# Optimization experiments

Measured on AMD Instinct MI355X. Metric: run time of the kernel, lower is better.

The kernel has to match this reference:

```python
import jax, jax.numpy as jnp
import numpy as np

G = 100000   # num graphs
N = 2000000  # num nodes
E = 4000000  # num edges (unused downstream, kept for fidelity)
D = 300      # emb_dim
L = 50       # num noise levels


def setup_inputs() -> dict:
    key = jax.random.key(0)
    ks = jax.random.split(key, 12)
    node2graph = jnp.sort(jax.random.randint(ks[0], (N,), 0, G))
    edge_index = jax.random.randint(ks[1], (2, E), 0, N)
    noise_level = jax.random.randint(ks[2], (G,), 0, L)
    molecule_repr = jax.random.normal(ks[3], (G, D), dtype=jnp.float32)
    pos_noise_pred = jax.random.normal(ks[4], (N, 3), dtype=jnp.float32)
    pos_perturbed = jax.random.normal(ks[5], (N, 3), dtype=jnp.float32)
    pos_target = jax.random.normal(ks[6], (N, 3), dtype=jnp.float32)
    s = 1.0 / np.sqrt(D)
    W1 = jax.random.uniform(ks[7], (D, D), minval=-s, maxval=s, dtype=jnp.float32)
    b1 = jax.random.uniform(ks[8], (D,), minval=-s, maxval=s, dtype=jnp.float32)
    W2 = jax.random.uniform(ks[9], (D, D), minval=-s, maxval=s, dtype=jnp.float32)
    b2 = jax.random.uniform(ks[10], (D,), minval=-s, maxval=s, dtype=jnp.float32)
    sigmas = jnp.asarray(np.exp(np.linspace(np.log(10.0), np.log(0.01), L)), dtype=jnp.float32)
    return dict(node2graph=node2graph, edge_index=edge_index, noise_level=noise_level,
                num_graphs=G, molecule_repr=molecule_repr, pos_noise_pred=pos_noise_pred,
                pos_perturbed=pos_perturbed, pos_target=pos_target,
                W1=W1, b1=b1, W2=W2, b2=b2, sigmas=sigmas)


def _score_target_riemann(pos_perturbed, pos_target, node2graph, num_graphs):
    # @torch.no_grad() branch: all scatter_mean/scatter_add indexed by node2graph
    seg_sum = lambda x: jax.ops.segment_sum(x, node2graph, num_segments=num_graphs)
    cnt = jnp.maximum(seg_sum(jnp.ones((node2graph.shape[0],), jnp.float32)), 1.0)[:, None]
    center = seg_sum(pos_target) / cnt                 # [G,3]
    p_center = seg_sum(pos_perturbed) / cnt            # [G,3]
    pos_c = pos_target - center[node2graph]            # [N,3]
    pp_c = pos_perturbed - p_center[node2graph]        # [N,3]
    # per-graph 3x3 matrices: ptp[i,j] = sum pp_i*pp_j, otp[i,j] = sum pos_c_i*pp_j
    ptp = seg_sum(pp_c[:, :, None] * pp_c[:, None, :])   # [G,3,3]
    otp = seg_sum(pos_c[:, :, None] * pp_c[:, None, :])  # [G,3,3]
    ptp_n = ptp[node2graph]                              # [N,3,3]
    otp_n = otp[node2graph]                              # [N,3,3]
    num = -2.0 * (jnp.einsum('ni,nij->nj', pp_c, ptp_n)
                  - jnp.einsum('ni,nij->nj', pos_c, otp_n))  # [N,3]
    den = (jnp.linalg.norm(ptp_n.reshape(-1, 9), axis=-1)
           + jnp.linalg.norm(otp_n.reshape(-1, 9), axis=-1))[:, None]
    return num / den


def reference(node2graph, edge_index, noise_level, num_graphs, molecule_repr,
              pos_noise_pred, pos_perturbed, pos_target, W1, b1, W2, b2, sigmas):
    edge2graph = node2graph[edge_index[0]]  # computed but unused, as in original
    used_sigmas = sigmas[noise_level][node2graph][:, None]  # [N,1]
    score_target = jax.lax.stop_gradient(
        _score_target_riemann(pos_perturbed, pos_target, node2graph, num_graphs)
    ) / used_sigmas
    pred_noise = (pos_noise_pred - pos_perturbed) * (1.0 / used_sigmas)
    per_node = jnp.sum((pred_noise - score_target) ** 2, axis=-1)  # [N]
    per_graph = jax.ops.segment_sum(per_node, node2graph, num_segments=num_graphs)
    pos_denoise = per_graph.mean()
    # noise-level prediction head: Linear -> SiLU -> Linear, CE over noise_level
    h = jax.nn.silu(molecule_repr @ W1 + b1)
    logits = h @ W2 + b2  # [G,D]
    logp = jax.nn.log_softmax(logits, axis=-1)
    ce = -jnp.take_along_axis(logp, noise_level[:, None], axis=1)[:, 0]
    loss_pred_noise = ce.mean()
    return jnp.stack([pos_denoise, loss_pred_noise])
```

## Files before the change

kernel.cpp:

```cpp
#include <hip/hip_runtime.h>
#include <math.h>


typedef __attribute__((ext_vector_type(8))) short bf16x8;
typedef __attribute__((ext_vector_type(4))) short s16x4;
typedef __attribute__((ext_vector_type(4))) float f32x4;

__device__ __forceinline__ short bt(float f) {
    return (short)(__float_as_uint(f) >> 16);
}

#define TM   64
#define DRL  300
#define DP   320
#define XS   328
#define NT   20
#define MT   4
#define KCH  10


__global__ __launch_bounds__(256)
void k_bnd(const int* __restrict__ n2g, int* __restrict__ gs,
           int* __restrict__ ge, int N) {
    int t = blockIdx.x * blockDim.x + threadIdx.x;
    if (t >= N) return;
    int g = n2g[t];
    if (t == 0     || n2g[t - 1] != g) gs[g] = t;
    if (t == N - 1 || n2g[t + 1] != g) ge[g] = t + 1;
}

__global__ __launch_bounds__(256)
void k_graph(const int* __restrict__ gs, const int* __restrict__ ge,
             const float* __restrict__ pt, const float* __restrict__ pp,
             const float* __restrict__ pnp,
             const int* __restrict__ nl, const float* __restrict__ sigmas,
             double* __restrict__ accA, int G) {
    const int tg = blockIdx.x * blockDim.x + threadIdx.x;
    const int g  = tg >> 2;
    const int j  = tg & 3;
    float q = 0.f;
    if (g < G) {
        const int s = gs[g], e = ge[g];
        float st0=0,st1=0,st2=0, sp0=0,sp1=0,sp2=0;
        float m00=0,m01=0,m02=0,m11=0,m12=0,m22=0;
        float t00=0,t01=0,t02=0,t10=0,t11=0,t12=0,t20=0,t21=0,t22=0;
        for (int i = s + j; i < e; i += 4) {
            float a0 = pt[3*i], a1 = pt[3*i+1], a2 = pt[3*i+2];
            float b0 = pp[3*i], b1 = pp[3*i+1], b2 = pp[3*i+2];
            st0 += a0; st1 += a1; st2 += a2;
            sp0 += b0; sp1 += b1; sp2 += b2;
            m00 += b0*b0; m01 += b0*b1; m02 += b0*b2;
            m11 += b1*b1; m12 += b1*b2; m22 += b2*b2;
            t00 += a0*b0; t01 += a0*b1; t02 += a0*b2;
            t10 += a1*b0; t11 += a1*b1; t12 += a1*b2;
            t20 += a2*b0; t21 += a2*b1; t22 += a2*b2;
        }
#define QR(x) do { x += __shfl_xor(x, 1, 64); x += __shfl_xor(x, 2, 64); } while (0)
        QR(st0); QR(st1); QR(st2); QR(sp0); QR(sp1); QR(sp2);
        QR(m00); QR(m01); QR(m02); QR(m11); QR(m12); QR(m22);
        QR(t00); QR(t01); QR(t02); QR(t10); QR(t11); QR(t12);
        QR(t20); QR(t21); QR(t22);
#undef QR
        float cnt = fmaxf((float)(e - s), 1.f);
        float ic  = 1.f / cnt;
        float c0 = st0 * ic, c1 = st1 * ic, c2 = st2 * ic;
        float d0 = sp0 * ic, d1 = sp1 * ic, d2 = sp2 * ic;
        float p00 = m00 - cnt*d0*d0, p01 = m01 - cnt*d0*d1;
        float p02 = m02 - cnt*d0*d2, p11 = m11 - cnt*d1*d1;
        float p12 = m12 - cnt*d1*d2, p22 = m22 - cnt*d2*d2;
        float o00 = t00 - cnt*c0*d0, o01 = t01 - cnt*c0*d1, o02 = t02 - cnt*c0*d2;
        float o10 = t10 - cnt*c1*d0, o11 = t11 - cnt*c1*d1, o12 = t12 - cnt*c1*d2;
        float o20 = t20 - cnt*c2*d0, o21 = t21 - cnt*c2*d1, o22 = t22 - cnt*c2*d2;
        float ptn = sqrtf(p00*p00 + p11*p11 + p22*p22 +
                          2.f*(p01*p01 + p02*p02 + p12*p12));
        float otn = sqrtf(o00*o00 + o01*o01 + o02*o02 +
                          o10*o10 + o11*o11 + o12*o12 +
                          o20*o20 + o21*o21 + o22*o22);
        float den = ptn + otn;
        float idn = (den > 0.f) ? (1.f / den) : 0.f;
        float sg  = sigmas[nl[g]];
        float is2 = 1.f / (sg * sg);
        for (int i = s + j; i < e; i += 4) {
            float a0 = pt[3*i] - c0, a1 = pt[3*i+1] - c1, a2 = pt[3*i+2] - c2;
            float bb0 = pp[3*i],  bb1 = pp[3*i+1],  bb2 = pp[3*i+2];
            float b0 = bb0 - d0, b1 = bb1 - d1, b2 = bb2 - d2;
            float n0 = -2.f * ((b0*p00 + b1*p01 + b2*p02) - (a0*o00 + a1*o10 + a2*o20));
            float n1 = -2.f * ((b0*p01 + b1*p11 + b2*p12) - (a0*o01 + a1*o11 + a2*o21));
            float n2 = -2.f * ((b0*p02 + b1*p12 + b2*p22) - (a0*o02 + a1*o12 + a2*o22));
            float e0 = (pnp[3*i]   - bb0) - n0 * idn;
            float e1 = (pnp[3*i+1] - bb1) - n1 * idn;
            float e2 = (pnp[3*i+2] - bb2) - n2 * idn;
            q += (e0*e0 + e1*e1 + e2*e2) * is2;
        }
    }
    for (int o = 32; o > 0; o >>= 1) q += __shfl_down(q, o, 64);
    if ((threadIdx.x & 63) == 0)
        atomicAdd(&accA[(blockIdx.x * 4 + (threadIdx.x >> 6)) & 255], (double)q);
}


__global__ void k_prepw(const float* __restrict__ W1, const float* __restrict__ W2,
                        short* __restrict__ Wb1, short* __restrict__ Wb2) {
    int id = blockIdx.x * blockDim.x + threadIdx.x;
    if (id >= 2 * DP * DP) return;
    int mat = id / (DP * DP);
    int rem = id - mat * DP * DP;
    int k = rem / DP, n = rem - (rem / DP) * DP;
    const float* W = mat ? W2 : W1;
    short* Wb = mat ? Wb2 : Wb1;
    float v = (k < DRL && n < DRL) ? W[k * DRL + n] : 0.f;
    int kc = k >> 5, kin = k & 31, quad = kin >> 3, j = kin & 7;
    int t = n >> 4, l16 = n & 15;
    Wb[(((kc * NT + t) * 64) + quad * 16 + l16) * 8 + j] = bt(v);
}


__global__ __launch_bounds__(640, 5)
void k_mlp(const float* __restrict__ X,
           const short* __restrict__ Wb1, const short* __restrict__ Wb2,
           const float* __restrict__ b1, const float* __restrict__ b2,
           const int* __restrict__ nl,
           double* __restrict__ accC, int G) {
    __shared__ __align__(16) short Xs[TM * XS];

    const int tid  = threadIdx.x;
    const int wv   = tid >> 6;
    const int lane = tid & 63;
    const int quad = lane >> 4;
    const int l16  = lane & 15;
    const int m0   = blockIdx.x * TM;

    const float4* Xv = (const float4*)X;
    for (int idx = tid; idx < TM * 75; idx += 640) {
        int r = idx / 75, c = idx - r * 75;
        int gr = m0 + r;
        float4 v = {0.f, 0.f, 0.f, 0.f};
        if (gr < G) v = Xv[gr * 75 + c];
        s16x4 sv = { bt(v.x), bt(v.y), bt(v.z), bt(v.w) };
        *(s16x4*)&Xs[r * XS + c * 4] = sv;
    }
    for (int idx = tid; idx < TM * (DP - DRL); idx += 640) {
        int r = idx / (DP - DRL), c = idx - r * (DP - DRL);
        Xs[r * XS + DRL + c] = 0;
    }
    __syncthreads();

    const bf16x8* B1 = (const bf16x8*)Wb1;
    const bf16x8* B2 = (const bf16x8*)Wb2;
    const int tile0 = wv * 2, tile1 = wv * 2 + 1;

    f32x4 acc[MT][2];
    const f32x4 vzero = {0.f, 0.f, 0.f, 0.f};
#pragma unroll
    for (int m = 0; m < MT; ++m) { acc[m][0] = vzero; acc[m][1] = vzero; }

    bf16x8 nb0 = B1[(0 * NT + tile0) * 64 + lane];
    bf16x8 nb1 = B1[(0 * NT + tile1) * 64 + lane];
#pragma unroll
    for (int kc = 0; kc < KCH; ++kc) {
        bf16x8 b0v = nb0, b1v = nb1;
        if (kc + 1 < KCH) {
            nb0 = B1[((kc + 1) * NT + tile0) * 64 + lane];
            nb1 = B1[((kc + 1) * NT + tile1) * 64 + lane];
        }
        bf16x8 a[MT];
#pragma unroll
        for (int m = 0; m < MT; ++m)
            a[m] = *(const bf16x8*)&Xs[(m * 16 + l16) * XS + kc * 32 + quad * 8];
#pragma unroll
        for (int m = 0; m < MT; ++m) {
            acc[m][0] = __builtin_amdgcn_mfma_f32_16x16x32_bf16(a[m], b0v, acc[m][0], 0, 0, 0);
            acc[m][1] = __builtin_amdgcn_mfma_f32_16x16x32_bf16(a[m], b1v, acc[m][1], 0, 0, 0);
        }
    }
    __syncthreads();

#pragma unroll
    for (int t = 0; t < 2; ++t) {
        int col = (wv * 2 + t) * 16 + l16;
        float bias = (col < DRL) ? b1[col] : 0.f;
#pragma unroll
        for (int m = 0; m < MT; ++m)
#pragma unroll
            for (int r = 0; r < 4; ++r) {
                float v = acc[m][t][r] + bias;
                float h = v / (1.f + __expf(-v));
                Xs[(m * 16 + quad * 4 + r) * XS + col] = bt(h);
            }
    }
    __syncthreads();

#pragma unroll
    for (int m = 0; m < MT; ++m) { acc[m][0] = vzero; acc[m][1] = vzero; }
    nb0 = B2[(0 * NT + tile0) * 64 + lane];
    nb1 = B2[(0 * NT + tile1) * 64 + lane];
#pragma unroll
    for (int kc = 0; kc < KCH; ++kc) {
        bf16x8 b0v = nb0, b1v = nb1;
        if (kc + 1 < KCH) {
            nb0 = B2[((kc + 1) * NT + tile0) * 64 + lane];
            nb1 = B2[((kc + 1) * NT + tile1) * 64 + lane];
        }
        bf16x8 a[MT];
#pragma unroll
        for (int m = 0; m < MT; ++m)
            a[m] = *(const bf16x8*)&Xs[(m * 16 + l16) * XS + kc * 32 + quad * 8];
#pragma unroll
        for (int m = 0; m < MT; ++m) {
            acc[m][0] = __builtin_amdgcn_mfma_f32_16x16x32_bf16(a[m], b0v, acc[m][0], 0, 0, 0);
            acc[m][1] = __builtin_amdgcn_mfma_f32_16x16x32_bf16(a[m], b1v, acc[m][1], 0, 0, 0);
        }
    }
    __syncthreads();

    float* S = (float*)Xs;
    float* T = S + TM * 10;
    const int colA = tile0 * 16 + l16;
    const int colB = tile1 * 16 + l16;
    const float biasA = (colA < DRL) ? b2[colA] : 0.f;
    const float biasB = (colB < DRL) ? b2[colB] : 0.f;
#pragma unroll
    for (int m = 0; m < MT; ++m) {
#pragma unroll
        for (int r = 0; r < 4; ++r) {
            int row = m * 16 + quad * 4 + r;
            int grow = m0 + row;
            int ct = (grow < G) ? nl[grow] : -1;
            float lgA = acc[m][0][r] + biasA;
            float lgB = acc[m][1][r] + biasB;
            float sw = ((colA < DRL) ? __expf(lgA) : 0.f) +
                       ((colB < DRL) ? __expf(lgB) : 0.f);
            for (int o = 1; o < 16; o <<= 1) sw += __shfl_xor(sw, o, 64);
            if (l16 == 0) S[row * 10 + wv] = sw;
            if (colA == ct) T[row] = lgA;
            if (colB == ct) T[row] = lgB;
        }
    }
    __syncthreads();
    if (tid < 64) {
        int row = tid;
        int grow = m0 + row;
        float q = 0.f;
        if (grow < G) {
            float ss = 0.f;
#pragma unroll
            for (int w = 0; w < 10; ++w) ss += S[row * 10 + w];
            q = __logf(ss) - T[row];
        }
        for (int o = 32; o > 0; o >>= 1) q += __shfl_down(q, o, 64);
        if (tid == 0) atomicAdd(&accC[blockIdx.x & 255], (double)q);
    }
}


__global__ void k_final(const double* __restrict__ accA,
                        const double* __restrict__ accC,
                        float* __restrict__ out, float invG) {
    int t = threadIdx.x;
    double a = accA[t] + accA[t + 64] + accA[t + 128] + accA[t + 192];
    double c = accC[t] + accC[t + 64] + accC[t + 128] + accC[t + 192];
    for (int o = 32; o > 0; o >>= 1) {
        a += __shfl_down(a, o, 64);
        c += __shfl_down(c, o, 64);
    }
    if (t == 0) {
        out[0] = (float)(a * (double)invG);
        out[1] = (float)(c * (double)invG);
    }
}


extern "C" void kernel_launch(void* const* d_in, const int* in_sizes, int n_in,
                              void* d_out, int out_size, void* d_ws, size_t ws_size,
                              hipStream_t stream) {
    const int*   n2g = (const int*)d_in[0];
    const int*   nl  = (const int*)d_in[2];
    const float* X   = (const float*)d_in[4];
    const float* pnp = (const float*)d_in[5];
    const float* pp  = (const float*)d_in[6];
    const float* pt  = (const float*)d_in[7];
    const float* W1  = (const float*)d_in[8];
    const float* b1  = (const float*)d_in[9];
    const float* W2  = (const float*)d_in[10];
    const float* b2  = (const float*)d_in[11];
    const float* sig = (const float*)d_in[12];

    const int N = in_sizes[0];
    const int G = in_sizes[2];

    double* accA = (double*)d_ws;
    double* accC = accA + 256;
    short*  Wb1  = (short*)((char*)d_ws + 4096);
    short*  Wb2  = Wb1 + DP * DP;
    int*    gs   = (int*)((char*)d_ws + 4096 + (size_t)2 * DP * DP * 2);
    int*    ge   = gs + G;

    hipMemsetAsync(d_ws, 0, 4096, stream);
    hipMemsetAsync(gs, 0, (size_t)2 * G * 4, stream);

    k_prepw<<<(2 * DP * DP + 255) / 256, 256, 0, stream>>>(W1, W2, Wb1, Wb2);
    k_bnd<<<(N + 255) / 256, 256, 0, stream>>>(n2g, gs, ge, N);
    k_graph<<<(4 * G + 255) / 256, 256, 0, stream>>>(gs, ge, pt, pp, pnp,
                                                     nl, sig, accA, G);
    k_mlp<<<(G + TM - 1) / TM, 640, 0, stream>>>(X, Wb1, Wb2, b1, b2, nl,
                                                 accC, G);
    k_final<<<1, 64, 0, stream>>>(accA, accC, (float*)d_out, 1.0f / (float)G);
}
```

Before: 395.2 us.

## Vectorize graph kernel loads and retile MLP to 32-row blocks of 4 waves

The per-graph kernel now loads positions as aligned float4 groups covering four nodes, masking nodes outside the graph, instead of strided scalar loads. The MLP kernel is retiled to 32-row blocks with 256 threads, where each wave computes five column tiles over two row tiles. The aims are better memory coalescing and higher occupancy. In exchange, weight traffic per row doubles and boundary groups are loaded redundantly.

```diff
diff --git a/kernel.cpp b/kernel.cpp
--- a/kernel.cpp
+++ b/kernel.cpp
@@ -10,12 +10,12 @@
     return (short)(__float_as_uint(f) >> 16);
 }
 
-#define TM   64
+#define TM   32
 #define DRL  300
 #define DP   320
 #define XS   328
 #define NT   20
-#define MT   4
+#define NW   5
 #define KCH  10
 
 
@@ -41,19 +41,39 @@
     float q = 0.f;
     if (g < G) {
         const int s = gs[g], e = ge[g];
+        const int g0 = s >> 2, g1 = (e + 3) >> 2;
+        const float4* ptv = (const float4*)pt;
+        const float4* ppv = (const float4*)pp;
+        const float4* pnv = (const float4*)pnp;
         float st0=0,st1=0,st2=0, sp0=0,sp1=0,sp2=0;
         float m00=0,m01=0,m02=0,m11=0,m12=0,m22=0;
         float t00=0,t01=0,t02=0,t10=0,t11=0,t12=0,t20=0,t21=0,t22=0;
-        for (int i = s + j; i < e; i += 4) {
-            float a0 = pt[3*i], a1 = pt[3*i+1], a2 = pt[3*i+2];
-            float b0 = pp[3*i], b1 = pp[3*i+1], b2 = pp[3*i+2];
-            st0 += a0; st1 += a1; st2 += a2;
-            sp0 += b0; sp1 += b1; sp2 += b2;
-            m00 += b0*b0; m01 += b0*b1; m02 += b0*b2;
-            m11 += b1*b1; m12 += b1*b2; m22 += b2*b2;
-            t00 += a0*b0; t01 += a0*b1; t02 += a0*b2;
-            t10 += a1*b0; t11 += a1*b1; t12 += a1*b2;
-            t20 += a2*b0; t21 += a2*b1; t22 += a2*b2;
+        for (int gg = g0 + j; gg < g1; gg += 4) {
+            float4 x0 = ptv[3*gg], x1 = ptv[3*gg+1], x2 = ptv[3*gg+2];
+            float4 y0 = ppv[3*gg], y1 = ppv[3*gg+1], y2 = ppv[3*gg+2];
+            float A[12] = {x0.x,x0.y,x0.z,x0.w, x1.x,x1.y,x1.z,x1.w,
+                           x2.x,x2.y,x2.z,x2.w};
+            float B[12] = {y0.x,y0.y,y0.z,y0.w, y1.x,y1.y,y1.z,y1.w,
+                           y2.x,y2.y,y2.z,y2.w};
+            const int base = gg * 4;
+#pragma unroll
+            for (int k = 0; k < 4; ++k) {
+                const int i = base + k;
+                const bool v = (i >= s) && (i < e);
+                float a0 = v ? A[3*k+0] : 0.f;
+                float a1 = v ? A[3*k+1] : 0.f;
+                float a2 = v ? A[3*k+2] : 0.f;
+                float b0 = v ? B[3*k+0] : 0.f;
+                float b1 = v ? B[3*k+1] : 0.f;
+                float b2 = v ? B[3*k+2] : 0.f;
+                st0 += a0; st1 += a1; st2 += a2;
+                sp0 += b0; sp1 += b1; sp2 += b2;
+                m00 += b0*b0; m01 += b0*b1; m02 += b0*b2;
+                m11 += b1*b1; m12 += b1*b2; m22 += b2*b2;
+                t00 += a0*b0; t01 += a0*b1; t02 += a0*b2;
+                t10 += a1*b0; t11 += a1*b1; t12 += a1*b2;
+                t20 += a2*b0; t21 += a2*b1; t22 += a2*b2;
+            }
         }
 #define QR(x) do { x += __shfl_xor(x, 1, 64); x += __shfl_xor(x, 2, 64); } while (0)
         QR(st0); QR(st1); QR(st2); QR(sp0); QR(sp1); QR(sp2);
@@ -80,17 +100,33 @@
         float idn = (den > 0.f) ? (1.f / den) : 0.f;
         float sg  = sigmas[nl[g]];
         float is2 = 1.f / (sg * sg);
-        for (int i = s + j; i < e; i += 4) {
-            float a0 = pt[3*i] - c0, a1 = pt[3*i+1] - c1, a2 = pt[3*i+2] - c2;
-            float bb0 = pp[3*i],  bb1 = pp[3*i+1],  bb2 = pp[3*i+2];
-            float b0 = bb0 - d0, b1 = bb1 - d1, b2 = bb2 - d2;
-            float n0 = -2.f * ((b0*p00 + b1*p01 + b2*p02) - (a0*o00 + a1*o10 + a2*o20));
-            float n1 = -2.f * ((b0*p01 + b1*p11 + b2*p12) - (a0*o01 + a1*o11 + a2*o21));
-            float n2 = -2.f * ((b0*p02 + b1*p12 + b2*p22) - (a0*o02 + a1*o12 + a2*o22));
-            float e0 = (pnp[3*i]   - bb0) - n0 * idn;
-            float e1 = (pnp[3*i+1] - bb1) - n1 * idn;
-            float e2 = (pnp[3*i+2] - bb2) - n2 * idn;
-            q += (e0*e0 + e1*e1 + e2*e2) * is2;
+        for (int gg = g0 + j; gg < g1; gg += 4) {
+            float4 x0 = ptv[3*gg], x1 = ptv[3*gg+1], x2 = ptv[3*gg+2];
+            float4 y0 = ppv[3*gg], y1 = ppv[3*gg+1], y2 = ppv[3*gg+2];
+            float4 z0 = pnv[3*gg], z1 = pnv[3*gg+1], z2 = pnv[3*gg+2];
+            float A[12] = {x0.x,x0.y,x0.z,x0.w, x1.x,x1.y,x1.z,x1.w,
+                           x2.x,x2.y,x2.z,x2.w};
+            float B[12] = {y0.x,y0.y,y0.z,y0.w, y1.x,y1.y,y1.z,y1.w,
+                           y2.x,y2.y,y2.z,y2.w};
+            float C[12] = {z0.x,z0.y,z0.z,z0.w, z1.x,z1.y,z1.z,z1.w,
+                           z2.x,z2.y,z2.z,z2.w};
+            const int base = gg * 4;
+#pragma unroll
+            for (int k = 0; k < 4; ++k) {
+                const int i = base + k;
+                const bool v = (i >= s) && (i < e);
+                float a0 = A[3*k+0] - c0, a1 = A[3*k+1] - c1, a2 = A[3*k+2] - c2;
+                float bb0 = B[3*k+0], bb1 = B[3*k+1], bb2 = B[3*k+2];
+                float b0 = bb0 - d0, b1 = bb1 - d1, b2 = bb2 - d2;
+                float n0 = -2.f * ((b0*p00 + b1*p01 + b2*p02) - (a0*o00 + a1*o10 + a2*o20));
+                float n1 = -2.f * ((b0*p01 + b1*p11 + b2*p12) - (a0*o01 + a1*o11 + a2*o21));
+                float n2 = -2.f * ((b0*p02 + b1*p12 + b2*p22) - (a0*o02 + a1*o12 + a2*o22));
+                float e0 = (C[3*k+0] - bb0) - n0 * idn;
+                float e1 = (C[3*k+1] - bb1) - n1 * idn;
+                float e2 = (C[3*k+2] - bb2) - n2 * idn;
+                float contrib = (e0*e0 + e1*e1 + e2*e2) * is2;
+                q += v ? contrib : 0.f;
+            }
         }
     }
     for (int o = 32; o > 0; o >>= 1) q += __shfl_down(q, o, 64);
@@ -115,7 +151,7 @@
 }
 
 
-__global__ __launch_bounds__(640, 5)
+__global__ __launch_bounds__(256, 4)
 void k_mlp(const float* __restrict__ X,
            const short* __restrict__ Wb1, const short* __restrict__ Wb2,
            const float* __restrict__ b1, const float* __restrict__ b2,
@@ -129,9 +165,10 @@
     const int quad = lane >> 4;
     const int l16  = lane & 15;
     const int m0   = blockIdx.x * TM;
+    const int tb0  = wv * NW;
 
     const float4* Xv = (const float4*)X;
-    for (int idx = tid; idx < TM * 75; idx += 640) {
+    for (int idx = tid; idx < TM * 75; idx += 256) {
         int r = idx / 75, c = idx - r * 75;
         int gr = m0 + r;
         float4 v = {0.f, 0.f, 0.f, 0.f};
@@ -139,7 +176,7 @@
         s16x4 sv = { bt(v.x), bt(v.y), bt(v.z), bt(v.w) };
         *(s16x4*)&Xs[r * XS + c * 4] = sv;
     }
-    for (int idx = tid; idx < TM * (DP - DRL); idx += 640) {
+    for (int idx = tid; idx < TM * (DP - DRL); idx += 256) {
         int r = idx / (DP - DRL), c = idx - r * (DP - DRL);
         Xs[r * XS + DRL + c] = 0;
     }
@@ -147,43 +184,48 @@
 
     const bf16x8* B1 = (const bf16x8*)Wb1;
     const bf16x8* B2 = (const bf16x8*)Wb2;
-    const int tile0 = wv * 2, tile1 = wv * 2 + 1;
-
-    f32x4 acc[MT][2];
+
+    f32x4 acc[2][NW];
     const f32x4 vzero = {0.f, 0.f, 0.f, 0.f};
 #pragma unroll
-    for (int m = 0; m < MT; ++m) { acc[m][0] = vzero; acc[m][1] = vzero; }
-
-    bf16x8 nb0 = B1[(0 * NT + tile0) * 64 + lane];
-    bf16x8 nb1 = B1[(0 * NT + tile1) * 64 + lane];
-#pragma unroll
-    for (int kc = 0; kc < KCH; ++kc) {
-        bf16x8 b0v = nb0, b1v = nb1;
-        if (kc + 1 < KCH) {
-            nb0 = B1[((kc + 1) * NT + tile0) * 64 + lane];
-            nb1 = B1[((kc + 1) * NT + tile1) * 64 + lane];
-        }
-        bf16x8 a[MT];
-#pragma unroll
-        for (int m = 0; m < MT; ++m)
-            a[m] = *(const bf16x8*)&Xs[(m * 16 + l16) * XS + kc * 32 + quad * 8];
-#pragma unroll
-        for (int m = 0; m < MT; ++m) {
-            acc[m][0] = __builtin_amdgcn_mfma_f32_16x16x32_bf16(a[m], b0v, acc[m][0], 0, 0, 0);
-            acc[m][1] = __builtin_amdgcn_mfma_f32_16x16x32_bf16(a[m], b1v, acc[m][1], 0, 0, 0);
-        }
-    }
-    __syncthreads();
-
-#pragma unroll
-    for (int t = 0; t < 2; ++t) {
-        int col = (wv * 2 + t) * 16 + l16;
+    for (int m = 0; m < 2; ++m)
+#pragma unroll
+        for (int n = 0; n < NW; ++n) acc[m][n] = vzero;
+
+    {
+        bf16x8 nb[NW];
+#pragma unroll
+        for (int n = 0; n < NW; ++n) nb[n] = B1[(0 * NT + tb0 + n) * 64 + lane];
+#pragma unroll
+        for (int kc = 0; kc < KCH; ++kc) {
+            bf16x8 bv[NW];
+#pragma unroll
+            for (int n = 0; n < NW; ++n) bv[n] = nb[n];
+            if (kc + 1 < KCH) {
+#pragma unroll
+                for (int n = 0; n < NW; ++n)
+                    nb[n] = B1[((kc + 1) * NT + tb0 + n) * 64 + lane];
+            }
+            bf16x8 a0 = *(const bf16x8*)&Xs[(l16) * XS + kc * 32 + quad * 8];
+            bf16x8 a1 = *(const bf16x8*)&Xs[(16 + l16) * XS + kc * 32 + quad * 8];
+#pragma unroll
+            for (int n = 0; n < NW; ++n) {
+                acc[0][n] = __builtin_amdgcn_mfma_f32_16x16x32_bf16(a0, bv[n], acc[0][n], 0, 0, 0);
+                acc[1][n] = __builtin_amdgcn_mfma_f32_16x16x32_bf16(a1, bv[n], acc[1][n], 0, 0, 0);
+            }
+        }
+    }
+    __syncthreads();
+
+#pragma unroll
+    for (int n = 0; n < NW; ++n) {
+        int col = (tb0 + n) * 16 + l16;
         float bias = (col < DRL) ? b1[col] : 0.f;
 #pragma unroll
-        for (int m = 0; m < MT; ++m)
+        for (int m = 0; m < 2; ++m)
 #pragma unroll
             for (int r = 0; r < 4; ++r) {
-                float v = acc[m][t][r] + bias;
+                float v = acc[m][n][r] + bias;
                 float h = v / (1.f + __expf(-v));
                 Xs[(m * 16 + quad * 4 + r) * XS + col] = bt(h);
             }
@@ -191,61 +233,65 @@
     __syncthreads();
 
 #pragma unroll
-    for (int m = 0; m < MT; ++m) { acc[m][0] = vzero; acc[m][1] = vzero; }
-    nb0 = B2[(0 * NT + tile0) * 64 + lane];
-    nb1 = B2[(0 * NT + tile1) * 64 + lane];
-#pragma unroll
-    for (int kc = 0; kc < KCH; ++kc) {
-        bf16x8 b0v = nb0, b1v = nb1;
-        if (kc + 1 < KCH) {
-            nb0 = B2[((kc + 1) * NT + tile0) * 64 + lane];
-            nb1 = B2[((kc + 1) * NT + tile1) * 64 + lane];
-        }
-        bf16x8 a[MT];
-#pragma unroll
-        for (int m = 0; m < MT; ++m)
-            a[m] = *(const bf16x8*)&Xs[(m * 16 + l16) * XS + kc * 32 + quad * 8];
-#pragma unroll
-        for (int m = 0; m < MT; ++m) {
-            acc[m][0] = __builtin_amdgcn_mfma_f32_16x16x32_bf16(a[m], b0v, acc[m][0], 0, 0, 0);
-            acc[m][1] = __builtin_amdgcn_mfma_f32_16x16x32_bf16(a[m], b1v, acc[m][1], 0, 0, 0);
+    for (int m = 0; m < 2; ++m)
+#pragma unroll
+        for (int n = 0; n < NW; ++n) acc[m][n] = vzero;
+    {
+        bf16x8 nb[NW];
+#pragma unroll
+        for (int n = 0; n < NW; ++n) nb[n] = B2[(0 * NT + tb0 + n) * 64 + lane];
+#pragma unroll
+        for (int kc = 0; kc < KCH; ++kc) {
+            bf16x8 bv[NW];
+#pragma unroll
+            for (int n = 0; n < NW; ++n) bv[n] = nb[n];
+            if (kc + 1 < KCH) {
+#pragma unroll
+                for (int n = 0; n < NW; ++n)
+                    nb[n] = B2[((kc + 1) * NT + tb0 + n) * 64 + lane];
+            }
+            bf16x8 a0 = *(const bf16x8*)&Xs[(l16) * XS + kc * 32 + quad * 8];
+            bf16x8 a1 = *(const bf16x8*)&Xs[(16 + l16) * XS + kc * 32 + quad * 8];
+#pragma unroll
+            for (int n = 0; n < NW; ++n) {
+                acc[0][n] = __builtin_amdgcn_mfma_f32_16x16x32_bf16(a0, bv[n], acc[0][n], 0, 0, 0);
+                acc[1][n] = __builtin_amdgcn_mfma_f32_16x16x32_bf16(a1, bv[n], acc[1][n], 0, 0, 0);
+            }
         }
     }
     __syncthreads();
 
     float* S = (float*)Xs;
-    float* T = S + TM * 10;
-    const int colA = tile0 * 16 + l16;
-    const int colB = tile1 * 16 + l16;
-    const float biasA = (colA < DRL) ? b2[colA] : 0.f;
-    const float biasB = (colB < DRL) ? b2[colB] : 0.f;
-#pragma unroll
-    for (int m = 0; m < MT; ++m) {
+    float* T = S + TM * 4;
+#pragma unroll
+    for (int m = 0; m < 2; ++m) {
 #pragma unroll
         for (int r = 0; r < 4; ++r) {
             int row = m * 16 + quad * 4 + r;
             int grow = m0 + row;
             int ct = (grow < G) ? nl[grow] : -1;
-            float lgA = acc[m][0][r] + biasA;
-            float lgB = acc[m][1][r] + biasB;
-            float sw = ((colA < DRL) ? __expf(lgA) : 0.f) +
-                       ((colB < DRL) ? __expf(lgB) : 0.f);
+            float sw = 0.f;
+#pragma unroll
+            for (int n = 0; n < NW; ++n) {
+                int col = (tb0 + n) * 16 + l16;
+                float lg = acc[m][n][r] + ((col < DRL) ? b2[col] : 0.f);
+                if (col < DRL) sw += __expf(lg);
+                if (col == ct) T[row] = lg;
+            }
             for (int o = 1; o < 16; o <<= 1) sw += __shfl_xor(sw, o, 64);
-            if (l16 == 0) S[row * 10 + wv] = sw;
-            if (colA == ct) T[row] = lgA;
-            if (colB == ct) T[row] = lgB;
+            if (l16 == 0) S[row * 4 + wv] = sw;
         }
     }
     __syncthreads();
     if (tid < 64) {
+        float q = 0.f;
         int row = tid;
-        int grow = m0 + row;
-        float q = 0.f;
-        if (grow < G) {
-            float ss = 0.f;
-#pragma unroll
-            for (int w = 0; w < 10; ++w) ss += S[row * 10 + w];
-            q = __logf(ss) - T[row];
+        if (row < TM) {
+            int grow = m0 + row;
+            if (grow < G) {
+                float ss = S[row*4+0] + S[row*4+1] + S[row*4+2] + S[row*4+3];
+                q = __logf(ss) - T[row];
+            }
         }
         for (int o = 32; o > 0; o >>= 1) q += __shfl_down(q, o, 64);
         if (tid == 0) atomicAdd(&accC[blockIdx.x & 255], (double)q);
@@ -302,7 +348,7 @@
     k_bnd<<<(N + 255) / 256, 256, 0, stream>>>(n2g, gs, ge, N);
     k_graph<<<(4 * G + 255) / 256, 256, 0, stream>>>(gs, ge, pt, pp, pnp,
                                                      nl, sig, accA, G);
-    k_mlp<<<(G + TM - 1) / TM, 640, 0, stream>>>(X, Wb1, Wb2, b1, b2, nl,
+    k_mlp<<<(G + TM - 1) / TM, 256, 0, stream>>>(X, Wb1, Wb2, b1, b2, nl,
                                                  accC, G);
     k_final<<<1, 64, 0, stream>>>(accA, accC, (float*)d_out, 1.0f / (float)G);
 }
```

Result: faster. 380.7 us (-3.7%).
